# Performance work log

Measured on AMD Instinct MI355X. Metric: run time of the kernel, lower is better.

Reference implementation:

```python
import jax, jax.numpy as jnp
import numpy as np

N_NODES = 50000
N_EDGES = 400000
F_IN = 128
F_EDGE = 32
F_HID = 32
N_HEADS = 4
N_LAYERS = 2


def _edge_softmax(alpha_raw, dst, num_nodes):
    # alpha_raw: (E, H). The original flattens (E,H,1) edge-major with segment id
    # dst[e] for EVERY head, so normalization runs over all incoming edges AND all
    # heads of a node (heads share one softmax). dim_size N*H in the original only
    # adds never-read empty segments, so N segments is numerically identical.
    node_max = jax.ops.segment_max(jnp.max(alpha_raw, axis=1), dst, num_segments=num_nodes)
    exp_a = jnp.exp(alpha_raw - node_max[dst][:, None])
    node_sum = jax.ops.segment_sum(jnp.sum(exp_a, axis=1), dst, num_segments=num_nodes)
    return exp_a / (node_sum[dst][:, None] + 1e-8)


def _layer(h, edge_attr, src, dst, p):
    # h: (N, H, F); edge_attr: (E, Fe); src=edge_index[0], dst=edge_index[1]
    (asw, asb, adw, adb, aew, aeb, dw, db, mdw, mdb, mew, meb, wnw, wnb) = p
    N, H, F = h.shape
    E = src.shape[0]
    xs = h @ asw + asb                       # attn_src(x): (N,H,F)
    xd = h @ adw + adb                       # attn_dst(x): (N,H,F)
    ea = edge_attr @ aew + aeb               # attn_edg(e): (E,F)
    attn_in = jax.nn.relu(xs[dst] + xd[src] + ea[:, None, :])   # (E,H,F)
    alpha_raw = (attn_in @ dw + db)[..., 0]                     # attn_dot: (E,H)
    alpha = _edge_softmax(alpha_raw, dst, N)                    # (E,H)
    xm = h @ mdw + mdb                       # msg_dst(x): (N,H,F)
    em = edge_attr @ mew + meb               # msg_edg(e): (E,F)
    msg = (alpha[..., None] * (xm[dst] + em[:, None, :])).reshape(E * H, F)
    # Original: edge_index.repeat(1, H) (head-tiled) paired with edge-major
    # (e,h)-flattened messages -> message k=e*H+h is scattered to dst[k mod E].
    idx = jnp.tile(dst, H)                   # (E*H,)
    aggr = jax.ops.segment_sum(msg, idx, num_segments=N * H).reshape(N, H, F)
    return aggr + (h @ wnw + wnb)            # + wgt_n(x)


def _forward(x, edge_attr, edge_index, atom_w, atom_b, layer_params):
    src, dst = edge_index[0], edge_index[1]
    N = x.shape[0]
    atom_in = jax.nn.relu((x @ atom_w + atom_b).reshape(N, N_HEADS, F_HID))
    h = atom_in
    for l in range(N_LAYERS):
        p = tuple(w[l] for w in layer_params)
        h = jax.nn.relu(_layer(h, edge_attr, src, dst, p) + atom_in)
    return h.mean(axis=1)                    # (N, F_HID)


def setup_inputs() -> dict:
    key = jax.random.key(0)
    ks = jax.random.split(key, 20)
    s = 0.05
    rn = lambda k, sh: jax.random.normal(k, sh, dtype=jnp.float32)
    L, F, Fe = N_LAYERS, F_HID, F_EDGE
    z = lambda sh: jnp.zeros(sh, jnp.float32)
    return {
        "x": rn(ks[0], (N_NODES, F_IN)),
        "edge_attr": rn(ks[1], (N_EDGES, Fe)),
        "edge_index": jax.random.randint(ks[2], (2, N_EDGES), 0, N_NODES, dtype=jnp.int32),
        "atom_w": rn(ks[3], (F_IN, F * N_HEADS)) * s,
        "atom_b": z((F * N_HEADS,)),
        "attn_src_w": rn(ks[4], (L, F, F)) * s, "attn_src_b": z((L, F)),
        "attn_dst_w": rn(ks[5], (L, F, F)) * s, "attn_dst_b": z((L, F)),
        "attn_edg_w": rn(ks[6], (L, Fe, F)) * s, "attn_edg_b": z((L, F)),
        "attn_dot_w": rn(ks[7], (L, F, 1)) * s, "attn_dot_b": z((L, 1)),
        "msg_dst_w": rn(ks[8], (L, F, F)) * s, "msg_dst_b": z((L, F)),
        "msg_edg_w": rn(ks[9], (L, Fe, F)) * s, "msg_edg_b": z((L, F)),
        "wgt_n_w": rn(ks[10], (L, F, F)) * s, "wgt_n_b": z((L, F)),
    }


def reference(x, edge_attr, edge_index, atom_w, atom_b, attn_src_w, attn_src_b,
              attn_dst_w, attn_dst_b, attn_edg_w, attn_edg_b, attn_dot_w, attn_dot_b,
              msg_dst_w, msg_dst_b, msg_edg_w, msg_edg_b, wgt_n_w, wgt_n_b):
    lp = (attn_src_w, attn_src_b, attn_dst_w, attn_dst_b, attn_edg_w, attn_edg_b,
          attn_dot_w, attn_dot_b, msg_dst_w, msg_dst_b, msg_edg_w, msg_edg_b,
          wgt_n_w, wgt_n_b)
    return _forward(x, edge_attr, edge_index, atom_w, atom_b, lp)
```

## Files before the change

kernel.cpp:

```cpp
#include <hip/hip_runtime.h>

#define N_NODES 50000
#define N_EDGES 400000
#define EQ      100000
#define F_IN    128
#define F_EDGE  32
#define F       32
#define H       4
#define NHF     128

#define SCAN_BLK 512
#define N_SCAN_BLKS ((N_NODES + SCAN_BLK - 1) / SCAN_BLK)

__device__ __forceinline__ float bf2f(unsigned short u) {
    return __uint_as_float(((unsigned)u) << 16);
}
__device__ __forceinline__ unsigned short f2bf(float f) {
    unsigned u = __float_as_uint(f);
    return (unsigned short)((u + 0x7FFFu + ((u >> 16) & 1u)) >> 16);
}
__device__ __forceinline__ ushort4 pack4(float4 v) {
    return make_ushort4(f2bf(v.x), f2bf(v.y), f2bf(v.z), f2bf(v.w));
}

__global__ __launch_bounds__(256) void k_atom(const float* __restrict__ x,
                                              const float* __restrict__ w,
                                              const float* __restrict__ b,
                                              float* __restrict__ out) {
    __shared__ float wlds[F_IN * NHF];
    __shared__ float xl[32 * F_IN];
    const float4* w4 = (const float4*)w;
    float4* wl4 = (float4*)wlds;
    for (int i = threadIdx.x; i < F_IN * NHF / 4; i += 256) wl4[i] = w4[i];
    int nb = blockIdx.x * 32;
    int nrows = min(32, N_NODES - nb);
    const float4* x4 = (const float4*)(x + (size_t)nb * F_IN);
    float4* xl4 = (float4*)xl;
    for (int i = threadIdx.x; i < nrows * F_IN / 4; i += 256) xl4[i] = x4[i];
    __syncthreads();
    int jg = threadIdx.x & 31;
    int nl = threadIdx.x >> 5;
    float4 bv = *(const float4*)(b + jg * 4);
    float4 acc[4] = {bv, bv, bv, bv};
    for (int k = 0; k < F_IN; k++) {
        float4 wv = *(const float4*)(wlds + k * NHF + jg * 4);
#pragma unroll
        for (int q = 0; q < 4; q++) {
            float xk = xl[(nl + 8 * q) * F_IN + k];
            acc[q].x += xk * wv.x; acc[q].y += xk * wv.y;
            acc[q].z += xk * wv.z; acc[q].w += xk * wv.w;
        }
    }
#pragma unroll
    for (int q = 0; q < 4; q++) {
        int n = nb + nl + 8 * q;
        if (n < N_NODES) {
            float4 a = acc[q];
            a.x = fmaxf(a.x, 0.f); a.y = fmaxf(a.y, 0.f);
            a.z = fmaxf(a.z, 0.f); a.w = fmaxf(a.w, 0.f);
            *(float4*)(out + (size_t)n * NHF + jg * 4) = a;
        }
    }
}

__global__ __launch_bounds__(256) void k_hist(const int* __restrict__ dst,
                                              int* __restrict__ counts) {
    int e = blockIdx.x * 256 + threadIdx.x;
    if (e < N_EDGES) atomicAdd(counts + dst[e], 1);
}

__global__ __launch_bounds__(SCAN_BLK) void k_scan1(const int* __restrict__ counts,
        int* __restrict__ excl, int* __restrict__ bsum) {
    __shared__ int s[SCAN_BLK];
    int i = blockIdx.x * SCAN_BLK + threadIdx.x;
    int v = (i < N_NODES) ? counts[i] : 0;
    s[threadIdx.x] = v;
    __syncthreads();
    for (int d = 1; d < SCAN_BLK; d <<= 1) {
        int t = (threadIdx.x >= d) ? s[threadIdx.x - d] : 0;
        __syncthreads();
        s[threadIdx.x] += t;
        __syncthreads();
    }
    if (i < N_NODES) excl[i] = s[threadIdx.x] - v;
    if (threadIdx.x == SCAN_BLK - 1) bsum[blockIdx.x] = s[SCAN_BLK - 1];
}

__global__ __launch_bounds__(128) void k_scan2(int* __restrict__ bsum) {
    __shared__ int s[128];
    int v = (threadIdx.x < N_SCAN_BLKS) ? bsum[threadIdx.x] : 0;
    s[threadIdx.x] = v;
    __syncthreads();
    for (int d = 1; d < 128; d <<= 1) {
        int t = (threadIdx.x >= d) ? s[threadIdx.x - d] : 0;
        __syncthreads();
        s[threadIdx.x] += t;
        __syncthreads();
    }
    if (threadIdx.x < N_SCAN_BLKS) bsum[threadIdx.x] = s[threadIdx.x] - v;
}

__global__ __launch_bounds__(SCAN_BLK) void k_scan3(const int* __restrict__ excl,
        const int* __restrict__ bsum, int* __restrict__ row_start,
        int* __restrict__ cursor) {
    int i = blockIdx.x * SCAN_BLK + threadIdx.x;
    if (i < N_NODES) {
        int v = excl[i] + bsum[blockIdx.x];
        row_start[i] = v;
        cursor[i] = v;
    }
}

__global__ __launch_bounds__(256) void k_fill(const int* __restrict__ src,
        const int* __restrict__ dst, int* __restrict__ cursor,
        int* __restrict__ csr_e, int* __restrict__ srcp,
        int* __restrict__ inv_pos) {
    int e = blockIdx.x * 256 + threadIdx.x;
    if (e < N_EDGES) {
        int pos = atomicAdd(cursor + dst[e], 1);
        csr_e[pos] = e;
        srcp[pos] = src[e];
        inv_pos[e] = pos;
    }
}

__global__ __launch_bounds__(256) void k_nodelin3(const float* __restrict__ h,
        const float* __restrict__ ws, const float* __restrict__ bs,
        const float* __restrict__ wd, const float* __restrict__ bd,
        const float* __restrict__ wm, const float* __restrict__ bm,
        unsigned short* __restrict__ xs, unsigned short* __restrict__ xd,
        unsigned short* __restrict__ xm) {
    __shared__ float Ws[F * F], Wd[F * F], Wm[F * F];
    __shared__ float hrt[F][64];
    for (int i = threadIdx.x; i < F * F; i += 256) {
        Ws[i] = ws[i]; Wd[i] = wd[i]; Wm[i] = wm[i];
    }
    int rbase = blockIdx.x * 64;
    for (int i = threadIdx.x; i < 512; i += 256) {
        int row = i >> 3, kq = i & 7;
        float4 v = *(const float4*)(h + (size_t)(rbase + row) * F + kq * 4);
        hrt[kq * 4 + 0][row] = v.x; hrt[kq * 4 + 1][row] = v.y;
        hrt[kq * 4 + 2][row] = v.z; hrt[kq * 4 + 3][row] = v.w;
    }
    __syncthreads();
    int rl = threadIdx.x >> 2;
    int jg = threadIdx.x & 3;
    float4 s0 = *(const float4*)(bs + jg * 8), s1 = *(const float4*)(bs + jg * 8 + 4);
    float4 d0 = *(const float4*)(bd + jg * 8), d1 = *(const float4*)(bd + jg * 8 + 4);
    float4 m0 = *(const float4*)(bm + jg * 8), m1 = *(const float4*)(bm + jg * 8 + 4);
    for (int k = 0; k < F; k++) {
        float hv = hrt[k][rl];
        float4 a, b2;
        a = *(const float4*)(Ws + k * F + jg * 8); b2 = *(const float4*)(Ws + k * F + jg * 8 + 4);
        s0.x += hv * a.x; s0.y += hv * a.y; s0.z += hv * a.z; s0.w += hv * a.w;
        s1.x += hv * b2.x; s1.y += hv * b2.y; s1.z += hv * b2.z; s1.w += hv * b2.w;
        a = *(const float4*)(Wd + k * F + jg * 8); b2 = *(const float4*)(Wd + k * F + jg * 8 + 4);
        d0.x += hv * a.x; d0.y += hv * a.y; d0.z += hv * a.z; d0.w += hv * a.w;
        d1.x += hv * b2.x; d1.y += hv * b2.y; d1.z += hv * b2.z; d1.w += hv * b2.w;
        a = *(const float4*)(Wm + k * F + jg * 8); b2 = *(const float4*)(Wm + k * F + jg * 8 + 4);
        m0.x += hv * a.x; m0.y += hv * a.y; m0.z += hv * a.z; m0.w += hv * a.w;
        m1.x += hv * b2.x; m1.y += hv * b2.y; m1.z += hv * b2.z; m1.w += hv * b2.w;
    }
    size_t o = (size_t)(rbase + rl) * F + jg * 8;
    *(ushort4*)(xs + o) = pack4(s0); *(ushort4*)(xs + o + 4) = pack4(s1);
    *(ushort4*)(xd + o) = pack4(d0); *(ushort4*)(xd + o + 4) = pack4(d1);
    *(ushort4*)(xm + o) = pack4(m0); *(ushort4*)(xm + o + 4) = pack4(m1);
}

__global__ __launch_bounds__(256) void k_edgepair(const float* __restrict__ edge_attr,
        const float* __restrict__ aew, const float* __restrict__ aeb,
        const float* __restrict__ mew, const float* __restrict__ meb,
        const int* __restrict__ inv_pos, unsigned short* __restrict__ ea_csr,
        unsigned short* __restrict__ emX) {
    __shared__ float Wa[F_EDGE * F], Wm2[F_EDGE * F];
    __shared__ float ert[F_EDGE][64];
    for (int i = threadIdx.x; i < F_EDGE * F; i += 256) {
        Wa[i] = aew[i]; Wm2[i] = mew[i];
    }
    int ebase = blockIdx.x * 64;
    for (int i = threadIdx.x; i < 512; i += 256) {
        int row = i >> 3, kq = i & 7;
        float4 v = *(const float4*)(edge_attr + (size_t)(ebase + row) * F_EDGE + kq * 4);
        ert[kq * 4 + 0][row] = v.x; ert[kq * 4 + 1][row] = v.y;
        ert[kq * 4 + 2][row] = v.z; ert[kq * 4 + 3][row] = v.w;
    }
    __syncthreads();
    int el = threadIdx.x >> 2;
    int jg = threadIdx.x & 3;
    float4 a0 = *(const float4*)(aeb + jg * 8), a1 = *(const float4*)(aeb + jg * 8 + 4);
    float4 m0 = *(const float4*)(meb + jg * 8), m1 = *(const float4*)(meb + jg * 8 + 4);
    for (int k = 0; k < F_EDGE; k++) {
        float ev = ert[k][el];
        float4 w0, w1;
        w0 = *(const float4*)(Wa + k * F + jg * 8); w1 = *(const float4*)(Wa + k * F + jg * 8 + 4);
        a0.x += ev * w0.x; a0.y += ev * w0.y; a0.z += ev * w0.z; a0.w += ev * w0.w;
        a1.x += ev * w1.x; a1.y += ev * w1.y; a1.z += ev * w1.z; a1.w += ev * w1.w;
        w0 = *(const float4*)(Wm2 + k * F + jg * 8); w1 = *(const float4*)(Wm2 + k * F + jg * 8 + 4);
        m0.x += ev * w0.x; m0.y += ev * w0.y; m0.z += ev * w0.z; m0.w += ev * w0.w;
        m1.x += ev * w1.x; m1.y += ev * w1.y; m1.z += ev * w1.z; m1.w += ev * w1.w;
    }
    int e = ebase + el;
    int p = inv_pos[e];
    size_t oa = (size_t)p * F + jg * 8;
    *(ushort4*)(ea_csr + oa) = pack4(a0);
    *(ushort4*)(ea_csr + oa + 4) = pack4(a1);
    int q = e % EQ, j = e / EQ;
    size_t om = (size_t)q * NHF + j * F + jg * 8;
    *(ushort4*)(emX + om) = pack4(m0);
    *(ushort4*)(emX + om + 4) = pack4(m1);
}

__global__ __launch_bounds__(256) void k_attn(const unsigned short* __restrict__ ea_csr,
        const unsigned short* __restrict__ xs, const unsigned short* __restrict__ xd,
        const int* __restrict__ srcp, const int* __restrict__ row_start,
        const int* __restrict__ counts, const int* __restrict__ csr_e,
        const float* __restrict__ dw, const float* __restrict__ db,
        float* __restrict__ alphaT) {
    __shared__ float lg[4][512];
    int wv = threadIdx.x >> 6, lane = threadIdx.x & 63;
    int n = blockIdx.x * 4 + wv;
    if (n >= N_NODES) return;
    int start = row_start[n];
    int items = counts[n] * 4;
    float4 wreg[8];
#pragma unroll
    for (int q = 0; q < 8; q++) wreg[q] = *(const float4*)(dw + q * 4);
    float dbv = db[0];
    const unsigned short* xsr = xs + (size_t)n * NHF;
    float m = -1e30f;
    for (int i = lane; i < items; i += 64) {
        int ii = i >> 2, hh = i & 3;
        int p = start + ii;
        int s = srcp[p];
        const unsigned short* ear = ea_csr + (size_t)p * F;
        const unsigned short* xsh = xsr + hh * F;
        const unsigned short* xdh = xd + (size_t)s * NHF + hh * F;
        float acc = 0.f;
#pragma unroll
        for (int q = 0; q < 8; q++) {
            ushort4 ue = *(const ushort4*)(ear + q * 4);
            ushort4 ua = *(const ushort4*)(xsh + q * 4);
            ushort4 ub = *(const ushort4*)(xdh + q * 4);
            acc += fmaxf(bf2f(ua.x) + bf2f(ub.x) + bf2f(ue.x), 0.f) * wreg[q].x;
            acc += fmaxf(bf2f(ua.y) + bf2f(ub.y) + bf2f(ue.y), 0.f) * wreg[q].y;
            acc += fmaxf(bf2f(ua.z) + bf2f(ub.z) + bf2f(ue.z), 0.f) * wreg[q].z;
            acc += fmaxf(bf2f(ua.w) + bf2f(ub.w) + bf2f(ue.w), 0.f) * wreg[q].w;
        }
        float l = acc + dbv;
        lg[wv][i] = l;
        m = fmaxf(m, l);
    }
#pragma unroll
    for (int d = 1; d < 64; d <<= 1) m = fmaxf(m, __shfl_xor(m, d));
    float ssum = 0.f;
    for (int i = lane; i < items; i += 64) ssum += __expf(lg[wv][i] - m);
#pragma unroll
    for (int d = 1; d < 64; d <<= 1) ssum += __shfl_xor(ssum, d);
    float inv = 1.f / (ssum + 1e-8f);
    for (int i = lane; i < items; i += 64) {
        int ii = i >> 2, hh = i & 3;
        int e = csr_e[start + ii];
        float a = __expf(lg[wv][i] - m) * inv;
        alphaT[(size_t)(e % EQ) * 16 + hh * 4 + (e / EQ)] = a;
    }
}

__global__ __launch_bounds__(256) void k_msgq(const float* __restrict__ alphaT,
        const unsigned short* __restrict__ emX, const unsigned short* __restrict__ xm,
        const int* __restrict__ dst, const int* __restrict__ inv_pos,
        unsigned short* __restrict__ ems_csr) {
    int g = blockIdx.x * 8 + (threadIdx.x >> 5);
    if (g >= EQ) return;
    int f = threadIdx.x & 31;
    const float4* a4 = (const float4*)(alphaT + (size_t)g * 16);
    float4 ac[4] = {a4[0], a4[1], a4[2], a4[3]};
    int4 dj = make_int4(dst[g], dst[g + EQ], dst[g + 2 * EQ], dst[g + 3 * EQ]);
    float out[4] = {0.f, 0.f, 0.f, 0.f};
#pragma unroll
    for (int j = 0; j < 4; j++) {
        int d = (j == 0) ? dj.x : (j == 1) ? dj.y : (j == 2) ? dj.z : dj.w;
        float emv = bf2f(emX[(size_t)g * NHF + j * F + f]);
        const unsigned short* xr = xm + (size_t)d * NHF + f;
#pragma unroll
        for (int c = 0; c < 4; c++) {
            float a = (j == 0) ? ac[c].x : (j == 1) ? ac[c].y
                    : (j == 2) ? ac[c].z : ac[c].w;
            out[c] += a * (bf2f(xr[c * F]) + emv);
        }
    }
    const int4 pos = *(const int4*)(inv_pos + (size_t)g * 4);
#pragma unroll
    for (int c = 0; c < 4; c++) {
        int p = (c == 0) ? pos.x : (c == 1) ? pos.y : (c == 2) ? pos.z : pos.w;
        ems_csr[(size_t)p * F + f] = f2bf(out[c]);
    }
}

__global__ __launch_bounds__(256) void k_combine(const float* __restrict__ h,
        const unsigned short* __restrict__ ems_csr, const int* __restrict__ row_start,
        const int* __restrict__ counts, const float* __restrict__ atom_in,
        const float* __restrict__ wn, const float* __restrict__ bn,
        float* __restrict__ hout, float* __restrict__ final_out, int is_final) {
    __shared__ float W[F * F];
    __shared__ float hrt[F][64];
    __shared__ float smv[64][F + 4];
    for (int i = threadIdx.x; i < F * F; i += 256) W[i] = wn[i];
    int rbase = blockIdx.x * 64;
    for (int i = threadIdx.x; i < 512; i += 256) {
        int row = i >> 3, kq = i & 7;
        float4 v = *(const float4*)(h + (size_t)(rbase + row) * F + kq * 4);
        hrt[kq * 4 + 0][row] = v.x; hrt[kq * 4 + 1][row] = v.y;
        hrt[kq * 4 + 2][row] = v.z; hrt[kq * 4 + 3][row] = v.w;
    }
    __syncthreads();
    int rl = threadIdx.x >> 2;
    int jg = threadIdx.x & 3;
    float4 a0 = *(const float4*)(bn + jg * 8);
    float4 a1 = *(const float4*)(bn + jg * 8 + 4);
    for (int k = 0; k < F; k++) {
        float hv = hrt[k][rl];
        float4 w0 = *(const float4*)(W + k * F + jg * 8);
        float4 w1 = *(const float4*)(W + k * F + jg * 8 + 4);
        a0.x += hv * w0.x; a0.y += hv * w0.y; a0.z += hv * w0.z; a0.w += hv * w0.w;
        a1.x += hv * w1.x; a1.y += hv * w1.y; a1.z += hv * w1.z; a1.w += hv * w1.w;
    }
    int m = rbase + rl;
    float4 g0 = make_float4(0.f, 0.f, 0.f, 0.f);
    float4 g1 = make_float4(0.f, 0.f, 0.f, 0.f);
    if (m < N_NODES) {
        int st = row_start[m], deg = counts[m];
        const unsigned short* er = ems_csr + (size_t)st * F + jg * 8;
        int p = 0;
        for (; p + 2 <= deg; p += 2) {
            ushort4 u0 = *(const ushort4*)(er);
            ushort4 u1 = *(const ushort4*)(er + 4);
            ushort4 v0 = *(const ushort4*)(er + F);
            ushort4 v1 = *(const ushort4*)(er + F + 4);
            g0.x += bf2f(u0.x) + bf2f(v0.x); g0.y += bf2f(u0.y) + bf2f(v0.y);
            g0.z += bf2f(u0.z) + bf2f(v0.z); g0.w += bf2f(u0.w) + bf2f(v0.w);
            g1.x += bf2f(u1.x) + bf2f(v1.x); g1.y += bf2f(u1.y) + bf2f(v1.y);
            g1.z += bf2f(u1.z) + bf2f(v1.z); g1.w += bf2f(u1.w) + bf2f(v1.w);
            er += 2 * F;
        }
        if (p < deg) {
            ushort4 u0 = *(const ushort4*)(er);
            ushort4 u1 = *(const ushort4*)(er + 4);
            g0.x += bf2f(u0.x); g0.y += bf2f(u0.y);
            g0.z += bf2f(u0.z); g0.w += bf2f(u0.w);
            g1.x += bf2f(u1.x); g1.y += bf2f(u1.y);
            g1.z += bf2f(u1.z); g1.w += bf2f(u1.w);
        }
    }
    size_t idx = (size_t)m * F + jg * 8;
    float4 t0 = *(const float4*)(atom_in + idx);
    float4 t1 = *(const float4*)(atom_in + idx + 4);
    float4 v0, v1;
    v0.x = fmaxf(a0.x + g0.x + t0.x, 0.f); v0.y = fmaxf(a0.y + g0.y + t0.y, 0.f);
    v0.z = fmaxf(a0.z + g0.z + t0.z, 0.f); v0.w = fmaxf(a0.w + g0.w + t0.w, 0.f);
    v1.x = fmaxf(a1.x + g1.x + t1.x, 0.f); v1.y = fmaxf(a1.y + g1.y + t1.y, 0.f);
    v1.z = fmaxf(a1.z + g1.z + t1.z, 0.f); v1.w = fmaxf(a1.w + g1.w + t1.w, 0.f);
    if (!is_final) {
        *(float4*)(hout + idx) = v0;
        *(float4*)(hout + idx + 4) = v1;
    } else {
        *(float4*)(&smv[rl][jg * 8]) = v0;
        *(float4*)(&smv[rl][jg * 8 + 4]) = v1;
        __syncthreads();
#pragma unroll
        for (int it = 0; it < 2; it++) {
            int oi = threadIdx.x + it * 256;
            int nl = oi >> 5, f = oi & 31;
            float o = 0.25f * (smv[nl * 4 + 0][f] + smv[nl * 4 + 1][f] +
                               smv[nl * 4 + 2][f] + smv[nl * 4 + 3][f]);
            final_out[((size_t)(rbase >> 2) + nl) * F + f] = o;
        }
    }
}

extern "C" void kernel_launch(void* const* d_in, const int* in_sizes, int n_in,
                              void* d_out, int out_size, void* d_ws, size_t ws_size,
                              hipStream_t stream) {
    const float* x         = (const float*)d_in[0];
    const float* edge_attr = (const float*)d_in[1];
    const int*   eidx      = (const int*)d_in[2];
    const int*   src       = eidx;
    const int*   dst       = eidx + N_EDGES;
    const float* atom_w    = (const float*)d_in[3];
    const float* atom_b    = (const float*)d_in[4];
    const float* asw = (const float*)d_in[5],  *asb = (const float*)d_in[6];
    const float* adw = (const float*)d_in[7],  *adb = (const float*)d_in[8];
    const float* aew = (const float*)d_in[9],  *aeb = (const float*)d_in[10];
    const float* dww = (const float*)d_in[11], *dwb = (const float*)d_in[12];
    const float* mdw = (const float*)d_in[13], *mdb = (const float*)d_in[14];
    const float* mew = (const float*)d_in[15], *meb = (const float*)d_in[16];
    const float* wnw = (const float*)d_in[17], *wnb = (const float*)d_in[18];
    float* out = (float*)d_out;

    float* ws = (float*)d_ws;
    size_t off = 0;
    float* atom_in = ws + off; off += (size_t)N_NODES * NHF;
    float* hbuf    = ws + off; off += (size_t)N_NODES * NHF;
    unsigned short* xs_bf  = (unsigned short*)(ws + off); off += (size_t)N_NODES * NHF / 2;
    unsigned short* xd_bf  = (unsigned short*)(ws + off); off += (size_t)N_NODES * NHF / 2;
    unsigned short* xm_bf  = (unsigned short*)(ws + off); off += (size_t)N_NODES * NHF / 2;
    unsigned short* ea_csr = (unsigned short*)(ws + off); off += (size_t)N_EDGES * F / 2;
    unsigned short* emX    = (unsigned short*)(ws + off); off += (size_t)N_EDGES * F / 2;
    unsigned short* ems    = (unsigned short*)(ws + off); off += (size_t)N_EDGES * F / 2;
    float* alphaT  = ws + off; off += (size_t)N_EDGES * H;
    int* counts    = (int*)(ws + off); off += N_NODES;
    int* row_start = (int*)(ws + off); off += N_NODES;
    int* cursor    = (int*)(ws + off); off += N_NODES;
    int* excl      = (int*)(ws + off); off += N_NODES;
    int* bsum      = (int*)(ws + off); off += 128;
    int* csr_e     = (int*)(ws + off); off += N_EDGES;
    int* srcp      = (int*)(ws + off); off += N_EDGES;
    int* inv_pos   = (int*)(ws + off); off += N_EDGES;

    hipMemsetAsync(counts, 0, N_NODES * sizeof(int), stream);
    k_hist <<<(N_EDGES + 255) / 256, 256, 0, stream>>>(dst, counts);
    k_scan1<<<N_SCAN_BLKS, SCAN_BLK, 0, stream>>>(counts, excl, bsum);
    k_scan2<<<1, 128, 0, stream>>>(bsum);
    k_scan3<<<N_SCAN_BLKS, SCAN_BLK, 0, stream>>>(excl, bsum, row_start, cursor);
    k_fill <<<(N_EDGES + 255) / 256, 256, 0, stream>>>(src, dst, cursor, csr_e,
                                                       srcp, inv_pos);

    k_atom<<<(N_NODES + 31) / 32, 256, 0, stream>>>(x, atom_w, atom_b, atom_in);

    for (int l = 0; l < 2; l++) {
        const float* hin  = (l == 0) ? atom_in : hbuf;
        float*       hout = hbuf;
        int is_final = (l == 1);
        k_nodelin3<<<(N_NODES * H) / 64, 256, 0, stream>>>(
            hin, asw + l * F * F, asb + l * F, adw + l * F * F, adb + l * F,
            mdw + l * F * F, mdb + l * F, xs_bf, xd_bf, xm_bf);
        k_edgepair<<<N_EDGES / 64, 256, 0, stream>>>(
            edge_attr, aew + l * F_EDGE * F, aeb + l * F,
            mew + l * F_EDGE * F, meb + l * F, inv_pos, ea_csr, emX);
        k_attn<<<(N_NODES + 3) / 4, 256, 0, stream>>>(
            ea_csr, xs_bf, xd_bf, srcp, row_start, counts, csr_e,
            dww + l * F, dwb + l, alphaT);
        k_msgq<<<(EQ + 7) / 8, 256, 0, stream>>>(alphaT, emX, xm_bf, dst,
                                                 inv_pos, ems);
        k_combine<<<(N_NODES * H) / 64, 256, 0, stream>>>(
            hin, ems, row_start, counts, atom_in, wnw + l * F * F,
            wnb + l * F, hout, out, is_final);
    }
}
```

Baseline: 583.4 us.

## Compute edge linear projections with bf16 MFMA and pre-packed edge attributes

Adds a one-time kernel that converts edge_attr to bf16 in MFMA A-fragment order, and rewrites the per-layer edge projection kernel to use 16x16x32 bf16 MFMA for both attention and message weights. Results are staged through per-wave LDS so that each row's 32 outputs are stored as 16-byte chunks to the CSR-permuted and head-tiled layouts. This aims to cut scalar FMA work and halve per-layer edge_attr reads, at the cost of an extra cast pass and bf16 rounding of the inputs and weights.

```diff
diff --git a/kernel.cpp b/kernel.cpp
--- a/kernel.cpp
+++ b/kernel.cpp
@@ -3,6 +3,7 @@
 #define N_NODES 50000
 #define N_EDGES 400000
 #define EQ      100000
+#define N_TILES 25000
 #define F_IN    128
 #define F_EDGE  32
 #define F       32
@@ -11,6 +12,9 @@
 
 #define SCAN_BLK 512
 #define N_SCAN_BLKS ((N_NODES + SCAN_BLK - 1) / SCAN_BLK)
+
+typedef __attribute__((ext_vector_type(8))) short bf16x8;
+typedef __attribute__((ext_vector_type(4))) float f32x4;
 
 __device__ __forceinline__ float bf2f(unsigned short u) {
     return __uint_as_float(((unsigned)u) << 16);
@@ -124,6 +128,75 @@
     }
 }
 
+__global__ __launch_bounds__(256) void k_cast(const float* __restrict__ edge_attr,
+                                              unsigned short* __restrict__ eaA) {
+    int t = blockIdx.x * 256 + threadIdx.x;
+    int tile = t >> 6, lane = t & 63;
+    int m = lane & 15, kq = lane >> 4;
+    const float4* s = (const float4*)(edge_attr + ((size_t)tile * 16 + m) * F_EDGE + kq * 8);
+    float4 v0 = s[0], v1 = s[1];
+    *(ushort4*)(eaA + (size_t)t * 8)     = pack4(v0);
+    *(ushort4*)(eaA + (size_t)t * 8 + 4) = pack4(v1);
+}
+
+__global__ __launch_bounds__(256) void k_edgepair(const unsigned short* __restrict__ eaA,
+        const float* __restrict__ aew, const float* __restrict__ aeb,
+        const float* __restrict__ mew, const float* __restrict__ meb,
+        const int* __restrict__ inv_pos, unsigned short* __restrict__ ea_csr,
+        unsigned short* __restrict__ emX) {
+    __shared__ unsigned short stg[4][2][16][40];
+    int wv = threadIdx.x >> 6, lane = threadIdx.x & 63;
+    int nn = lane & 15, kq = lane >> 4;
+    bf16x8 Ba0, Ba1, Bm0, Bm1;
+#pragma unroll
+    for (int j = 0; j < 8; j++) {
+        int k = kq * 8 + j;
+        Ba0[j] = (short)f2bf(aew[k * F + nn]);
+        Ba1[j] = (short)f2bf(aew[k * F + 16 + nn]);
+        Bm0[j] = (short)f2bf(mew[k * F + nn]);
+        Bm1[j] = (short)f2bf(mew[k * F + 16 + nn]);
+    }
+    float ba0 = aeb[nn], ba1 = aeb[16 + nn];
+    float bm0 = meb[nn], bm1 = meb[16 + nn];
+    for (int tt = 0; tt < 4; tt++) {
+        int tile = blockIdx.x * 16 + wv * 4 + tt;
+        if (tile >= N_TILES) break;
+        bf16x8 A = *(const bf16x8*)(eaA + ((size_t)tile * 64 + lane) * 8);
+        f32x4 c0 = {ba0, ba0, ba0, ba0};
+        f32x4 c1 = {ba1, ba1, ba1, ba1};
+        f32x4 c2 = {bm0, bm0, bm0, bm0};
+        f32x4 c3 = {bm1, bm1, bm1, bm1};
+        c0 = __builtin_amdgcn_mfma_f32_16x16x32_bf16(A, Ba0, c0, 0, 0, 0);
+        c1 = __builtin_amdgcn_mfma_f32_16x16x32_bf16(A, Ba1, c1, 0, 0, 0);
+        c2 = __builtin_amdgcn_mfma_f32_16x16x32_bf16(A, Bm0, c2, 0, 0, 0);
+        c3 = __builtin_amdgcn_mfma_f32_16x16x32_bf16(A, Bm1, c3, 0, 0, 0);
+#pragma unroll
+        for (int r = 0; r < 4; r++) {
+            int row = kq * 4 + r;
+            stg[wv][0][row][nn]      = f2bf(c0[r]);
+            stg[wv][0][row][nn + 16] = f2bf(c1[r]);
+            stg[wv][1][row][nn]      = f2bf(c2[r]);
+            stg[wv][1][row][nn + 16] = f2bf(c3[r]);
+        }
+        __builtin_amdgcn_s_waitcnt(0);
+#pragma unroll
+        for (int it = 0; it < 2; it++) {
+            int rg = (it == 0) ? (lane >> 2) : (16 + (lane >> 2));
+            int seg = lane & 3;
+            int mat = rg >> 4, r = rg & 15;
+            int e = tile * 16 + r;
+            uint4 v = *(uint4*)&stg[wv][mat][r][seg * 8];
+            if (mat == 0) {
+                int p = inv_pos[e];
+                *(uint4*)(ea_csr + (size_t)p * F + seg * 8) = v;
+            } else {
+                int q = e % EQ, j = e / EQ;
+                *(uint4*)(emX + (size_t)q * NHF + j * F + seg * 8) = v;
+            }
+        }
+    }
+}
+
 __global__ __launch_bounds__(256) void k_nodelin3(const float* __restrict__ h,
         const float* __restrict__ ws, const float* __restrict__ bs,
         const float* __restrict__ wd, const float* __restrict__ bd,
@@ -167,49 +240,6 @@
     *(ushort4*)(xm + o) = pack4(m0); *(ushort4*)(xm + o + 4) = pack4(m1);
 }
 
-__global__ __launch_bounds__(256) void k_edgepair(const float* __restrict__ edge_attr,
-        const float* __restrict__ aew, const float* __restrict__ aeb,
-        const float* __restrict__ mew, const float* __restrict__ meb,
-        const int* __restrict__ inv_pos, unsigned short* __restrict__ ea_csr,
-        unsigned short* __restrict__ emX) {
-    __shared__ float Wa[F_EDGE * F], Wm2[F_EDGE * F];
-    __shared__ float ert[F_EDGE][64];
-    for (int i = threadIdx.x; i < F_EDGE * F; i += 256) {
-        Wa[i] = aew[i]; Wm2[i] = mew[i];
-    }
-    int ebase = blockIdx.x * 64;
-    for (int i = threadIdx.x; i < 512; i += 256) {
-        int row = i >> 3, kq = i & 7;
-        float4 v = *(const float4*)(edge_attr + (size_t)(ebase + row) * F_EDGE + kq * 4);
-        ert[kq * 4 + 0][row] = v.x; ert[kq * 4 + 1][row] = v.y;
-        ert[kq * 4 + 2][row] = v.z; ert[kq * 4 + 3][row] = v.w;
-    }
-    __syncthreads();
-    int el = threadIdx.x >> 2;
-    int jg = threadIdx.x & 3;
-    float4 a0 = *(const float4*)(aeb + jg * 8), a1 = *(const float4*)(aeb + jg * 8 + 4);
-    float4 m0 = *(const float4*)(meb + jg * 8), m1 = *(const float4*)(meb + jg * 8 + 4);
-    for (int k = 0; k < F_EDGE; k++) {
-        float ev = ert[k][el];
-        float4 w0, w1;
-        w0 = *(const float4*)(Wa + k * F + jg * 8); w1 = *(const float4*)(Wa + k * F + jg * 8 + 4);
-        a0.x += ev * w0.x; a0.y += ev * w0.y; a0.z += ev * w0.z; a0.w += ev * w0.w;
-        a1.x += ev * w1.x; a1.y += ev * w1.y; a1.z += ev * w1.z; a1.w += ev * w1.w;
-        w0 = *(const float4*)(Wm2 + k * F + jg * 8); w1 = *(const float4*)(Wm2 + k * F + jg * 8 + 4);
-        m0.x += ev * w0.x; m0.y += ev * w0.y; m0.z += ev * w0.z; m0.w += ev * w0.w;
-        m1.x += ev * w1.x; m1.y += ev * w1.y; m1.z += ev * w1.z; m1.w += ev * w1.w;
-    }
-    int e = ebase + el;
-    int p = inv_pos[e];
-    size_t oa = (size_t)p * F + jg * 8;
-    *(ushort4*)(ea_csr + oa) = pack4(a0);
-    *(ushort4*)(ea_csr + oa + 4) = pack4(a1);
-    int q = e % EQ, j = e / EQ;
-    size_t om = (size_t)q * NHF + j * F + jg * 8;
-    *(ushort4*)(emX + om) = pack4(m0);
-    *(ushort4*)(emX + om + 4) = pack4(m1);
-}
-
 __global__ __launch_bounds__(256) void k_attn(const unsigned short* __restrict__ ea_csr,
         const unsigned short* __restrict__ xs, const unsigned short* __restrict__ xd,
         const int* __restrict__ srcp, const int* __restrict__ row_start,
@@ -406,6 +436,7 @@
     unsigned short* ea_csr = (unsigned short*)(ws + off); off += (size_t)N_EDGES * F / 2;
     unsigned short* emX    = (unsigned short*)(ws + off); off += (size_t)N_EDGES * F / 2;
     unsigned short* ems    = (unsigned short*)(ws + off); off += (size_t)N_EDGES * F / 2;
+    unsigned short* eaA    = (unsigned short*)(ws + off); off += (size_t)N_EDGES * F_EDGE / 2;
     float* alphaT  = ws + off; off += (size_t)N_EDGES * H;
     int* counts    = (int*)(ws + off); off += N_NODES;
     int* row_start = (int*)(ws + off); off += N_NODES;
@@ -423,6 +454,7 @@
     k_scan3<<<N_SCAN_BLKS, SCAN_BLK, 0, stream>>>(excl, bsum, row_start, cursor);
     k_fill <<<(N_EDGES + 255) / 256, 256, 0, stream>>>(src, dst, cursor, csr_e,
                                                        srcp, inv_pos);
+    k_cast <<<(N_TILES * 64) / 256, 256, 0, stream>>>(edge_attr, eaA);
 
     k_atom<<<(N_NODES + 31) / 32, 256, 0, stream>>>(x, atom_w, atom_b, atom_in);
 
@@ -433,8 +465,8 @@
         k_nodelin3<<<(N_NODES * H) / 64, 256, 0, stream>>>(
             hin, asw + l * F * F, asb + l * F, adw + l * F * F, adb + l * F,
             mdw + l * F * F, mdb + l * F, xs_bf, xd_bf, xm_bf);
-        k_edgepair<<<N_EDGES / 64, 256, 0, stream>>>(
-            edge_attr, aew + l * F_EDGE * F, aeb + l * F,
+        k_edgepair<<<(N_TILES + 15) / 16, 256, 0, stream>>>(
+            eaA, aew + l * F_EDGE * F, aeb + l * F,
             mew + l * F_EDGE * F, meb + l * F, inv_pos, ea_csr, emX);
         k_attn<<<(N_NODES + 3) / 4, 256, 0, stream>>>(
             ea_csr, xs_bf, xd_bf, srcp, row_start, counts, csr_e,
```

Result: faster. 552.7 us (-5.3%).
